# Performance work log

Hardware: AMD Instinct MI355X
Metric: run time of the kernel (lower is better)

The kernel has to match this reference:

```python
import jax, jax.numpy as jnp
import numpy as np

CUTOFF = 10.0
EPS_W = 1e-5
EPS_LN = 1e-5

def _silu(v):
    return v * jax.nn.sigmoid(v)

def setup_inputs() -> dict:
    key = jax.random.key(0)
    ks = jax.random.split(key, 12)
    N, E, H, R = 50000, 300000, 256, 64
    s = lambda fan_in: 1.0 / np.sqrt(fan_in)
    inp = {
        'x': jax.random.normal(ks[0], (N, H), jnp.float32),
        'edge_index': jax.random.randint(ks[1], (2, E), 0, N, jnp.int64 if jax.config.jax_enable_x64 else jnp.int32),
        'distances': jax.random.uniform(ks[2], (E,), jnp.float32) * CUTOFF,
        'centers': jnp.linspace(0.0, CUTOFF, R).astype(jnp.float32),
        'widths': jnp.full((R,), CUTOFF / R, jnp.float32),
        'rbf_w1': jax.random.normal(ks[3], (R, R), jnp.float32) * s(R),
        'rbf_b1': jnp.zeros((R,), jnp.float32),
        'rbf_w2': jax.random.normal(ks[4], (R, R), jnp.float32) * s(R),
        'rbf_b2': jnp.zeros((R,), jnp.float32),
        'filt_w1': jax.random.normal(ks[5], (R, H), jnp.float32) * s(R),
        'filt_b1': jnp.zeros((H,), jnp.float32),
        'filt_w2': jax.random.normal(ks[6], (H, H), jnp.float32) * s(H),
        'filt_b2': jnp.zeros((H,), jnp.float32),
        'filt_w3': jax.random.normal(ks[7], (H, H), jnp.float32) * s(H),
        'filt_b3': jnp.zeros((H,), jnp.float32),
        'node_w': jax.random.normal(ks[8], (H, H), jnp.float32) * s(H),
        'node_b': jnp.zeros((H,), jnp.float32),
        'ln_g': jnp.ones((H,), jnp.float32),
        'ln_b': jnp.zeros((H,), jnp.float32),
        'gate_w': jax.random.normal(ks[9], (H, H), jnp.float32) * s(H),
        'gate_b': jnp.zeros((H,), jnp.float32),
    }
    return inp

def reference(x, edge_index, distances, centers, widths,
              rbf_w1, rbf_b1, rbf_w2, rbf_b2,
              filt_w1, filt_b1, filt_w2, filt_b2, filt_w3, filt_b3,
              node_w, node_b, ln_g, ln_b, gate_w, gate_b):
    # LearnableRBF: envelope * gaussian basis, then 2-layer SiLU proj
    d = distances
    env = 0.5 * (jnp.cos(d * jnp.pi / CUTOFF) + 1.0) * (d < CUTOFF).astype(x.dtype)  # [E]
    rbf = jnp.exp(-0.5 * ((d[:, None] - centers) / (jnp.abs(widths) + EPS_W)) ** 2)   # [E,R]
    r = rbf * env[:, None]
    r = _silu(r @ rbf_w1 + rbf_b1) @ rbf_w2 + rbf_b2                                  # [E,R]
    # filter network: Lin-SiLU-Lin-SiLU-Lin
    W = _silu(r @ filt_w1 + filt_b1)
    W = _silu(W @ filt_w2 + filt_b2) @ filt_w3 + filt_b3                              # [E,H]
    # gather -> modulate -> scatter-add (CFConv messaging)
    row, col = edge_index[0], edge_index[1]
    msg = (x[col] @ node_w + node_b) * W                                              # [E,H]
    agg = jax.ops.segment_sum(msg, row, num_segments=x.shape[0])                      # [N,H]
    h = x + agg
    mu = jnp.mean(h, axis=-1, keepdims=True)
    var = jnp.var(h, axis=-1, keepdims=True)
    out = (h - mu) / jnp.sqrt(var + EPS_LN) * ln_g + ln_b
    return out * jax.nn.sigmoid(out @ gate_w + gate_b)
```

## Files before the change

### kernel.cpp

```cpp
#include <hip/hip_runtime.h>
#include <hip/hip_bf16.h>
#include <math.h>

typedef __attribute__((ext_vector_type(8))) short bf16x8;
typedef __attribute__((ext_vector_type(4))) float f32x4;
typedef unsigned short ushort_t;

constexpr float F_CUTOFF = 10.0f;
constexpr float F_EPS_W  = 1e-5f;
constexpr float F_EPS_LN = 1e-5f;
constexpr float F_PI     = 3.14159265358979323846f;

__device__ __forceinline__ float silu_f(float v)   { return v / (1.0f + __expf(-v)); }
__device__ __forceinline__ float sigmoid_f(float v){ return 1.0f / (1.0f + __expf(-v)); }

__device__ __forceinline__ ushort_t f2bf(float f) {
    union { __hip_bfloat16 h; ushort_t u; } v; v.h = __float2bfloat16(f); return v.u;
}
__device__ __forceinline__ float bf2f(ushort_t u) {
    union { unsigned u; float f; } v; v.u = ((unsigned)u) << 16; return v.f;
}

__global__ void count_kernel(const int* __restrict__ eidx, int* __restrict__ cnt, int E)
{
// ... 160 lines not shown
    float4 bv1 = reinterpret_cast<const float4*>(bias)[j04 + 1];
    float bb[8] = {bv0.x, bv0.y, bv0.z, bv0.w, bv1.x, bv1.y, bv1.z, bv1.w};

    #pragma unroll
    for (int r = 0; r < 8; ++r) {
        int row = row0 + r0 + r;
        if (row >= M) continue;
        ushort_t o8[8];
        #pragma unroll
        for (int c = 0; c < 8; ++c) o8[c] = f2bf(acc[r][c] + bb[c]);
        *reinterpret_cast<uint4*>(out + (size_t)row * 256 + jt * 8) = *reinterpret_cast<uint4*>(o8);
    }
}

__global__ __launch_bounds__(256)
void gate_gemm_kernel(const float* __restrict__ A, const float* __restrict__ Wm,
                      const float* __restrict__ bias, float* __restrict__ out, int M)
{
    __shared__ float4 As4[64][64];
    const int t = threadIdx.x;
    const int row0 = blockIdx.x * 64;

    #pragma unroll
    for (int i = 0; i < 16; ++i) {
        int flat = t + i * 256;
        int r = flat >> 6, k4 = flat & 63;
        int row = row0 + r;
        float4 v = make_float4(0.f, 0.f, 0.f, 0.f);
        if (row < M) v = reinterpret_cast<const float4*>(A)[row * 64 + k4];
        As4[r][k4] = v;
    }
    __syncthreads();

    const int jt  = t & 31;
    const int et  = t >> 5;
    const int j04 = jt * 2;
    const int r0  = et * 8;

    float acc[8][8];
    #pragma unroll
    for (int r = 0; r < 8; ++r)
        #pragma unroll
        for (int c = 0; c < 8; ++c) acc[r][c] = 0.f;

    for (int k4 = 0; k4 < 64; ++k4) {
        float4 a4[8];
        #pragma unroll
        for (int r = 0; r < 8; ++r) a4[r] = As4[r0 + r][k4];
        #pragma unroll
        for (int q = 0; q < 4; ++q) {
            const int k = k4 * 4 + q;
            float4 b0 = reinterpret_cast<const float4*>(Wm)[k * 64 + j04];
            float4 b1 = reinterpret_cast<const float4*>(Wm)[k * 64 + j04 + 1];
            float bb[8] = {b0.x, b0.y, b0.z, b0.w, b1.x, b1.y, b1.z, b1.w};
            float av;
            #pragma unroll
            for (int r = 0; r < 8; ++r) {
                av = (q == 0) ? a4[r].x : (q == 1) ? a4[r].y : (q == 2) ? a4[r].z : a4[r].w;
                #pragma unroll
                for (int c = 0; c < 8; ++c) acc[r][c] = fmaf(av, bb[c], acc[r][c]);
            }
        }
    }

    float4 bv0 = reinterpret_cast<const float4*>(bias)[j04];
    float4 bv1 = reinterpret_cast<const float4*>(bias)[j04 + 1];
    float bb[8] = {bv0.x, bv0.y, bv0.z, bv0.w, bv1.x, bv1.y, bv1.z, bv1.w};

    #pragma unroll
    for (int r = 0; r < 8; ++r) {
        int row = row0 + r0 + r;
        if (row >= M) continue;
        float4 a0 = As4[r0 + r][j04];
        float4 a1 = As4[r0 + r][j04 + 1];
        float aa[8] = {a0.x, a0.y, a0.z, a0.w, a1.x, a1.y, a1.z, a1.w};
        float o[8];
        #pragma unroll
        for (int c = 0; c < 8; ++c) o[c] = aa[c] * sigmoid_f(acc[r][c] + bb[c]);
        reinterpret_cast<float4*>(out)[row * 64 + j04]     = make_float4(o[0], o[1], o[2], o[3]);
        reinterpret_cast<float4*>(out)[row * 64 + j04 + 1] = make_float4(o[4], o[5], o[6], o[7]);
    }
}

__global__ __launch_bounds__(256)
void rbf_kernel(const float* __restrict__ distp,
                const float* __restrict__ centers, const float* __restrict__ widths,
                ushort_t* __restrict__ r, int Mc)
{
    int idx = blockIdx.x * 256 + threadIdx.x;
    if (idx >= Mc * 8) return;
    int e  = idx >> 3;
    int c0 = (idx & 7) * 8;
    float d = distp[e];
    float env = (d < F_CUTOFF) ? 0.5f * (__cosf(d * (F_PI / F_CUTOFF)) + 1.0f) : 0.0f;
    ushort_t o[8];
    #pragma unroll
    for (int i = 0; i < 8; ++i) {
        int n = c0 + i;
        float w = fabsf(widths[n]) + F_EPS_W;
        float z = (d - centers[n]) / w;
        o[i] = f2bf(env * __expf(-0.5f * z * z));
    }
    *reinterpret_cast<uint4*>(r + (size_t)e * 64 + c0) = *reinterpret_cast<uint4*>(o);
}

__global__ __launch_bounds__(256, 4)
void gemm_k64_kernel(const ushort_t* A, const ushort_t* __restrict__ Wt,
                     const float* __restrict__ bias, ushort_t* out, int M)
{
    __shared__ __align__(16) unsigned char sA[128 * 128];
    const int t = threadIdx.x;
    const int m0 = blockIdx.x * 128;
    const int w = t >> 6, lane = t & 63;
    const int g = lane >> 4, q = lane & 15;

    #pragma unroll
    for (int i = 0; i < 4; ++i) {
        int s = t + i * 256;
        int r = s >> 3, u = s & 7;
        int row = m0 + r; row = (row < M) ? row : (M - 1);
        uint4 v = *reinterpret_cast<const uint4*>(A + (size_t)row * 64 + ((u ^ (r & 7)) * 8));
        *reinterpret_cast<uint4*>(sA + s * 16) = v;
    }
    __syncthreads();

    f32x4 acc[2][4];
    #pragma unroll
    for (int mt = 0; mt < 2; ++mt)
        #pragma unroll
        for (int nt = 0; nt < 4; ++nt) acc[mt][nt] = (f32x4){0.f, 0.f, 0.f, 0.f};

    #pragma unroll
    for (int kk = 0; kk < 2; ++kk) {
        bf16x8 b[4];
        #pragma unroll
        for (int nt = 0; nt < 4; ++nt) {
            int n = nt * 16 + q;
            b[nt] = *reinterpret_cast<const bf16x8*>(Wt + n * 64 + kk * 32 + g * 8);
        }
        bf16x8 a[2];
        #pragma unroll
        for (int mt = 0; mt < 2; ++mt) {
            int m = w * 32 + mt * 16 + q;
            int unit = (4 * kk + g) ^ (m & 7);
            a[mt] = *reinterpret_cast<const bf16x8*>(sA + m * 128 + unit * 16);
        }
        #pragma unroll
        for (int mt = 0; mt < 2; ++mt)
            #pragma unroll
            for (int nt = 0; nt < 4; ++nt)
                acc[mt][nt] = __builtin_amdgcn_mfma_f32_16x16x32_bf16(a[mt], b[nt], acc[mt][nt], 0, 0, 0);
    }
    __syncthreads();

    const bool evenq = (q & 1) == 0;
    #pragma unroll
    for (int nt = 0; nt < 4; ++nt) {
        int n0  = nt * 16 + q;
        int n_e = n0 & ~1;
        float2 bv = *reinterpret_cast<const float2*>(bias + n_e);
        #pragma unroll
        for (int mt = 0; mt < 2; ++mt) {
            float v[4], p[4];
            #pragma unroll
            for (int r = 0; r < 4; ++r) { v[r] = acc[mt][nt][r]; p[r] = __shfl_xor(v[r], 1, 64); }
            #pragma unroll
            for (int rr = 0; rr < 2; ++rr) {
                int r = evenq ? rr : (2 + rr);
                float lo = silu_f((evenq ? v[r] : p[r]) + bv.x);
                float hi = silu_f((evenq ? p[r] : v[r]) + bv.y);
                int m = w * 32 + mt * 16 + 4 * g + r;
                unsigned u = (unsigned)f2bf(lo) | ((unsigned)f2bf(hi) << 16);
                *reinterpret_cast<unsigned*>(sA + m * 128 + n_e * 2) = u;
            }
        }
    }
    __syncthreads();

    {
        int row = t >> 1, j = t & 1;
        if (m0 + row < M) {
            #pragma unroll
            for (int i = 0; i < 4; ++i) {
                uint4 v = *reinterpret_cast<const uint4*>(sA + row * 128 + (j * 4 + i) * 16);
                *reinterpret_cast<uint4*>(out + (size_t)(m0 + row) * 64 + (j * 4 + i) * 8) = v;
            }
        }
    }
}

__global__ __launch_bounds__(256, 4)
void gemm_k64n256_kernel(const ushort_t* __restrict__ A, const ushort_t* __restrict__ Wt,
                         const float* __restrict__ bias, ushort_t* __restrict__ out, int M)
{
    __shared__ __align__(16) unsigned char sA[64 * 128];
    __shared__ __align__(16) unsigned char obuf[32 * 512];
    const int t = threadIdx.x;
    const int m0 = blockIdx.x * 64;
    const int wn = t >> 6, lane = t & 63;
    const int g = lane >> 4, q = lane & 15;

    #pragma unroll
    for (int i = 0; i < 2; ++i) {
        int s = t + i * 256;
        int r = s >> 3, u = s & 7;
        int row = m0 + r; row = (row < M) ? row : (M - 1);
        uint4 v = *reinterpret_cast<const uint4*>(A + (size_t)row * 64 + ((u ^ (r & 7)) * 8));
        *reinterpret_cast<uint4*>(sA + s * 16) = v;
    }
    __syncthreads();

    f32x4 acc[4][4];
    #pragma unroll
    for (int mt = 0; mt < 4; ++mt)
        #pragma unroll
        for (int nt = 0; nt < 4; ++nt) acc[mt][nt] = (f32x4){0.f, 0.f, 0.f, 0.f};

    #pragma unroll
    for (int kk = 0; kk < 2; ++kk) {
        bf16x8 b[4];
        #pragma unroll
        for (int nt = 0; nt < 4; ++nt) {
            int n = wn * 64 + nt * 16 + q;
            b[nt] = *reinterpret_cast<const bf16x8*>(Wt + n * 64 + kk * 32 + g * 8);
        }
        bf16x8 a[4];
        #pragma unroll
        for (int mt = 0; mt < 4; ++mt) {
            int m = mt * 16 + q;
            int unit = (4 * kk + g) ^ (m & 7);
            a[mt] = *reinterpret_cast<const bf16x8*>(sA + m * 128 + unit * 16);
        }
        #pragma unroll
        for (int mt = 0; mt < 4; ++mt)
            #pragma unroll
            for (int nt = 0; nt < 4; ++nt)
                acc[mt][nt] = __builtin_amdgcn_mfma_f32_16x16x32_bf16(a[mt], b[nt], acc[mt][nt], 0, 0, 0);
    }

    const bool evenq = (q & 1) == 0;
    #pragma unroll
    for (int half = 0; half < 2; ++half) {
        #pragma unroll
        for (int mtl = 0; mtl < 2; ++mtl) {
            int mt = half * 2 + mtl;
            #pragma unroll
            for (int nt = 0; nt < 4; ++nt) {
                int n0  = wn * 64 + nt * 16 + q;
                int n_e = n0 & ~1;
                float2 bv = *reinterpret_cast<const float2*>(bias + n_e);
                float v[4], p[4];
                #pragma unroll
                for (int r = 0; r < 4; ++r) { v[r] = acc[mt][nt][r]; p[r] = __shfl_xor(v[r], 1, 64); }
                #pragma unroll
                for (int rr = 0; rr < 2; ++rr) {
                    int r = evenq ? rr : (2 + rr);
                    float lo = silu_f((evenq ? v[r] : p[r]) + bv.x);
                    float hi = silu_f((evenq ? p[r] : v[r]) + bv.y);
                    int ml = mtl * 16 + 4 * g + r;
                    unsigned u = (unsigned)f2bf(lo) | ((unsigned)f2bf(hi) << 16);
                    *reinterpret_cast<unsigned*>(obuf + ml * 512 + n_e * 2) = u;
                }
            }
        }
        __syncthreads();
        {
            int row = t >> 3, c = t & 7;
            int grow = m0 + half * 32 + row;
            if (grow < M) {
                #pragma unroll
                for (int i = 0; i < 4; ++i) {
                    uint4 v = *reinterpret_cast<const uint4*>(obuf + row * 512 + (c + 8 * i) * 16);
                    *reinterpret_cast<uint4*>(out + (size_t)grow * 256 + (c + 8 * i) * 8) = v;
                }
            }
        }
        __syncthreads();
    }
}

template<bool SILU>
__global__ __launch_bounds__(256, 3)
void gemm_k256_kernel(const ushort_t* __restrict__ A, const ushort_t* __restrict__ Wt,
                      const float* __restrict__ bias, ushort_t* __restrict__ out, int M)
{
    __shared__ __align__(16) unsigned char sbuf[2][8192];

    const int t  = threadIdx.x;
    const int m0 = blockIdx.x * 64;
    const int wn   = t >> 6;
    const int lane = t & 63;
    const int g = lane >> 4, q = lane & 15;

    const int s0r = t >> 3,         s0u = t & 7;
    const int s1r = (t + 256) >> 3, s1u = t & 7;
    const ushort_t* src0base = A + (size_t)((m0 + s0r < M) ? (m0 + s0r) : (M - 1)) * 256 + ((s0u ^ (s0r & 7)) * 8);
    const ushort_t* src1base = A + (size_t)((m0 + s1r < M) ? (m0 + s1r) : (M - 1)) * 256 + ((s1u ^ (s1r & 7)) * 8);

    uint4 p0 = *reinterpret_cast<const uint4*>(src0base);
    uint4 p1 = *reinterpret_cast<const uint4*>(src1base);
    *reinterpret_cast<uint4*>(&sbuf[0][t * 16])         = p0;
    *reinterpret_cast<uint4*>(&sbuf[0][(t + 256) * 16]) = p1;
    __syncthreads();

    f32x4 acc[4][4];
    #pragma unroll
    for (int mt = 0; mt < 4; ++mt)
        #pragma unroll
        for (int nt = 0; nt < 4; ++nt) acc[mt][nt] = (f32x4){0.f, 0.f, 0.f, 0.f};

    for (int kt = 0; kt < 4; ++kt) {
        const int cur = kt & 1;
        uint4 nx0, nx1;
        if (kt < 3) {
            nx0 = *reinterpret_cast<const uint4*>(src0base + (kt + 1) * 64);
            nx1 = *reinterpret_cast<const uint4*>(src1base + (kt + 1) * 64);
        }
        #pragma unroll
        for (int ks = 0; ks < 2; ++ks) {
            bf16x8 b[4];
            #pragma unroll
            for (int nt = 0; nt < 4; ++nt) {
                int n = wn * 64 + nt * 16 + q;
                b[nt] = *reinterpret_cast<const bf16x8*>(Wt + (size_t)n * 256 + kt * 64 + ks * 32 + g * 8);
            }
            bf16x8 a[4];
            #pragma unroll
            for (int mt = 0; mt < 4; ++mt) {
                int r = mt * 16 + q;
                int u = (ks * 4 + g) ^ (r & 7);
                a[mt] = *reinterpret_cast<const bf16x8*>(&sbuf[cur][r * 128 + u * 16]);
            }
            #pragma unroll
            for (int mt = 0; mt < 4; ++mt)
                #pragma unroll
                for (int nt = 0; nt < 4; ++nt)
                    acc[mt][nt] = __builtin_amdgcn_mfma_f32_16x16x32_bf16(a[mt], b[nt], acc[mt][nt], 0, 0, 0);
        }
        __syncthreads();
        if (kt < 3) {
            *reinterpret_cast<uint4*>(&sbuf[cur ^ 1][t * 16])         = nx0;
            *reinterpret_cast<uint4*>(&sbuf[cur ^ 1][(t + 256) * 16]) = nx1;
            __syncthreads();
        }
    }

    unsigned char* obuf = &sbuf[0][0];
    const bool evenq = (q & 1) == 0;
    #pragma unroll
    for (int half = 0; half < 2; ++half) {
        __syncthreads();
        #pragma unroll
        for (int mtl = 0; mtl < 2; ++mtl) {
            int mt = half * 2 + mtl;
            #pragma unroll
            for (int nt = 0; nt < 4; ++nt) {
                int n0  = wn * 64 + nt * 16 + q;
                int n_e = n0 & ~1;
                float2 bv = *reinterpret_cast<const float2*>(bias + n_e);
                float v[4], p[4];
                #pragma unroll
                for (int r = 0; r < 4; ++r) { v[r] = acc[mt][nt][r]; p[r] = __shfl_xor(v[r], 1, 64); }
                #pragma unroll
                for (int rr = 0; rr < 2; ++rr) {
                    int r = evenq ? rr : (2 + rr);
// ... 41 lines not shown

    uint4 p0 = *reinterpret_cast<const uint4*>(src0base);
    uint4 p1 = *reinterpret_cast<const uint4*>(src1base);
    *reinterpret_cast<uint4*>(&sbuf[0][t * 16])         = p0;
    *reinterpret_cast<uint4*>(&sbuf[0][(t + 256) * 16]) = p1;
    __syncthreads();

    f32x4 acc[4][4];
    #pragma unroll
    for (int mt = 0; mt < 4; ++mt)
        #pragma unroll
        for (int nt = 0; nt < 4; ++nt) acc[mt][nt] = (f32x4){0.f, 0.f, 0.f, 0.f};

    for (int kt = 0; kt < 4; ++kt) {
        const int cur = kt & 1;
        uint4 nx0, nx1;
        if (kt < 3) {
            nx0 = *reinterpret_cast<const uint4*>(src0base + (kt + 1) * 64);
            nx1 = *reinterpret_cast<const uint4*>(src1base + (kt + 1) * 64);
        }
        #pragma unroll
        for (int ks = 0; ks < 2; ++ks) {
            bf16x8 b[4];
            #pragma unroll
            for (int nt = 0; nt < 4; ++nt) {
                int n = wn * 64 + nt * 16 + q;
                b[nt] = *reinterpret_cast<const bf16x8*>(Wt + (size_t)n * 256 + kt * 64 + ks * 32 + g * 8);
            }
            bf16x8 a[4];
            #pragma unroll
            for (int mt = 0; mt < 4; ++mt) {
                int r = mt * 16 + q;
                int u = (ks * 4 + g) ^ (r & 7);
                a[mt] = *reinterpret_cast<const bf16x8*>(&sbuf[cur][r * 128 + u * 16]);
            }
            #pragma unroll
            for (int mt = 0; mt < 4; ++mt)
                #pragma unroll
                for (int nt = 0; nt < 4; ++nt)
                    acc[mt][nt] = __builtin_amdgcn_mfma_f32_16x16x32_bf16(a[mt], b[nt], acc[mt][nt], 0, 0, 0);
        }
        __syncthreads();
        if (kt < 3) {
            *reinterpret_cast<uint4*>(&sbuf[cur ^ 1][t * 16])         = nx0;
            *reinterpret_cast<uint4*>(&sbuf[cur ^ 1][(t + 256) * 16]) = nx1;
            __syncthreads();
        }
    }

    float bn[4];
    #pragma unroll
    for (int nt = 0; nt < 4; ++nt) bn[nt] = bias[wn * 64 + nt * 16 + q];

    #pragma unroll
    for (int p = 0; p < 4; ++p) {
        #pragma unroll
        for (int nt = 0; nt < 4; ++nt) {
            int col = wn * 64 + nt * 16 + q;
            #pragma unroll
            for (int r = 0; r < 4; ++r) {
                int rl = 4 * g + r;
                obuf[rl][col] = sigmoid_f(acc[p][nt][r] + bn[nt]);
            }
        }
        __syncthreads();
        {
            int rl = t >> 4, c16 = t & 15;
            int grow = m0 + p * 16 + rl;
            if (grow < M) {
                float* orow = out + (size_t)grow * 256 + c16 * 16;
                #pragma unroll
                for (int i = 0; i < 4; ++i) {
                    float4 g4 = *reinterpret_cast<const float4*>(&obuf[rl][c16 * 16 + i * 4]);
                    float4 a4 = *reinterpret_cast<const float4*>(orow + i * 4);
                    a4.x *= g4.x; a4.y *= g4.y; a4.z *= g4.z; a4.w *= g4.w;
                    *reinterpret_cast<float4*>(orow + i * 4) = a4;
                }
            }
        }
        __syncthreads();
    }
}

__global__ __launch_bounds__(256, 3)
void fused_de_kernel(const ushort_t* A, const ushort_t* __restrict__ Wt2,
                     const float* __restrict__ b2,
                     const ushort_t* __restrict__ Wt3, const float* __restrict__ b3,
                     ushort_t* out, int M)
{
    __shared__ __align__(16) unsigned char sbuf[2][8192];
    __shared__ __align__(16) unsigned char f2l[64 * 512];

    const int t  = threadIdx.x;
    const int m0 = blockIdx.x * 64;
    const int wn   = t >> 6;
    const int lane = t & 63;
    const int g = lane >> 4, q = lane & 15;

    const int s0r = t >> 3,         s0u = t & 7;
    const int s1r = (t + 256) >> 3, s1u = t & 7;
    const ushort_t* src0base = A + (size_t)((m0 + s0r < M) ? (m0 + s0r) : (M - 1)) * 256 + ((s0u ^ (s0r & 7)) * 8);
    const ushort_t* src1base = A + (size_t)((m0 + s1r < M) ? (m0 + s1r) : (M - 1)) * 256 + ((s1u ^ (s1r & 7)) * 8);

    uint4 p0 = *reinterpret_cast<const uint4*>(src0base);
    uint4 p1 = *reinterpret_cast<const uint4*>(src1base);
    *reinterpret_cast<uint4*>(&sbuf[0][t * 16])         = p0;
    *reinterpret_cast<uint4*>(&sbuf[0][(t + 256) * 16]) = p1;
    __syncthreads();

    f32x4 acc[4][4];
    #pragma unroll
    for (int mt = 0; mt < 4; ++mt)
        #pragma unroll
        for (int nt = 0; nt < 4; ++nt) acc[mt][nt] = (f32x4){0.f, 0.f, 0.f, 0.f};

    for (int kt = 0; kt < 4; ++kt) {
        const int cur = kt & 1;
        uint4 nx0, nx1;
        if (kt < 3) {
            nx0 = *reinterpret_cast<const uint4*>(src0base + (kt + 1) * 64);
            nx1 = *reinterpret_cast<const uint4*>(src1base + (kt + 1) * 64);
        }
        #pragma unroll
        for (int ks = 0; ks < 2; ++ks) {
            bf16x8 b[4];
            #pragma unroll
            for (int nt = 0; nt < 4; ++nt) {
                int n = wn * 64 + nt * 16 + q;
                b[nt] = *reinterpret_cast<const bf16x8*>(Wt2 + (size_t)n * 256 + kt * 64 + ks * 32 + g * 8);
            }
            bf16x8 a[4];
            #pragma unroll
            for (int mt = 0; mt < 4; ++mt) {
                int r = mt * 16 + q;
                int u = (ks * 4 + g) ^ (r & 7);
                a[mt] = *reinterpret_cast<const bf16x8*>(&sbuf[cur][r * 128 + u * 16]);
            }
            #pragma unroll
            for (int mt = 0; mt < 4; ++mt)
                #pragma unroll
                for (int nt = 0; nt < 4; ++nt)
                    acc[mt][nt] = __builtin_amdgcn_mfma_f32_16x16x32_bf16(a[mt], b[nt], acc[mt][nt], 0, 0, 0);
        }
        __syncthreads();
        if (kt < 3) {
            *reinterpret_cast<uint4*>(&sbuf[cur ^ 1][t * 16])         = nx0;
            *reinterpret_cast<uint4*>(&sbuf[cur ^ 1][(t + 256) * 16]) = nx1;
            __syncthreads();
        }
    }

    const bool evenq = (q & 1) == 0;
    #pragma unroll
    for (int nt = 0; nt < 4; ++nt) {
        int n0  = wn * 64 + nt * 16 + q;
        int n_e = n0 & ~1;
        float2 bv = *reinterpret_cast<const float2*>(b2 + n_e);
        #pragma unroll
        for (int mt = 0; mt < 4; ++mt) {
            float v[4], p[4];
            #pragma unroll
            for (int r = 0; r < 4; ++r) { v[r] = acc[mt][nt][r]; p[r] = __shfl_xor(v[r], 1, 64); }
            #pragma unroll
            for (int rr = 0; rr < 2; ++rr) {
                int r = evenq ? rr : (2 + rr);
                float lo = silu_f((evenq ? v[r] : p[r]) + bv.x);
                float hi = silu_f((evenq ? p[r] : v[r]) + bv.y);
                int m = mt * 16 + 4 * g + r;
                unsigned u = (unsigned)f2bf(lo) | ((unsigned)f2bf(hi) << 16);
                int byte = m * 512 + (((n_e >> 3) ^ (m & 7)) << 4) + ((n_e & 7) * 2);
                *reinterpret_cast<unsigned*>(f2l + byte) = u;
            }
        }
    }
    __syncthreads();

    #pragma unroll
    for (int mt = 0; mt < 4; ++mt)
        #pragma unroll
        for (int nt = 0; nt < 4; ++nt) acc[mt][nt] = (f32x4){0.f, 0.f, 0.f, 0.f};

    #pragma unroll
    for (int kk = 0; kk < 8; ++kk) {
        bf16x8 b[4];
        #pragma unroll
        for (int nt = 0; nt < 4; ++nt) {
            int n = wn * 64 + nt * 16 + q;
            b[nt] = *reinterpret_cast<const bf16x8*>(Wt3 + (size_t)n * 256 + kk * 32 + g * 8);
        }
        bf16x8 a[4];
        #pragma unroll
        for (int mt = 0; mt < 4; ++mt) {
            int m = mt * 16 + q;
            int unit = (4 * kk + g) ^ (m & 7);
            a[mt] = *reinterpret_cast<const bf16x8*>(f2l + m * 512 + unit * 16);
        }
        #pragma unroll
        for (int mt = 0; mt < 4; ++mt)
            #pragma unroll
            for (int nt = 0; nt < 4; ++nt)
                acc[mt][nt] = __builtin_amdgcn_mfma_f32_16x16x32_bf16(a[mt], b[nt], acc[mt][nt], 0, 0, 0);
    }

    unsigned char* obuf = &sbuf[0][0];
    #pragma unroll
    for (int half = 0; half < 2; ++half) {
        __syncthreads();
        #pragma unroll
        for (int mtl = 0; mtl < 2; ++mtl) {
            int mt = half * 2 + mtl;
            #pragma unroll
            for (int nt = 0; nt < 4; ++nt) {
                int n0  = wn * 64 + nt * 16 + q;
                int n_e = n0 & ~1;
                float2 bv = *reinterpret_cast<const float2*>(b3 + n_e);
                float v[4], p[4];
                #pragma unroll
                for (int r = 0; r < 4; ++r) { v[r] = acc[mt][nt][r]; p[r] = __shfl_xor(v[r], 1, 64); }
                #pragma unroll
                for (int rr = 0; rr < 2; ++rr) {
                    int r = evenq ? rr : (2 + rr);
                    float lo = (evenq ? v[r] : p[r]) + bv.x;
                    float hi = (evenq ? p[r] : v[r]) + bv.y;
                    int ml = mtl * 16 + 4 * g + r;
                    unsigned u = (unsigned)f2bf(lo) | ((unsigned)f2bf(hi) << 16);
                    *reinterpret_cast<unsigned*>(obuf + ml * 512 + n_e * 2) = u;
                }
            }
        }
        __syncthreads();
        {
            int row = t >> 3, c = t & 7;
            int grow = m0 + half * 32 + row;
            if (grow < M) {
                #pragma unroll
                for (int i = 0; i < 4; ++i) {
                    uint4 v = *reinterpret_cast<const uint4*>(obuf + row * 512 + (c + 8 * i) * 16);
                    *reinterpret_cast<uint4*>(out + (size_t)grow * 256 + (c + 8 * i) * 8) = v;
                }
            }
        }
    }
}

__global__ __launch_bounds__(256)
void agg_node_kernel(const ushort_t* __restrict__ Wf, const int* __restrict__ colp,
                     const int* __restrict__ start, const ushort_t* __restrict__ y,
                     float* __restrict__ agg, int cs, int ce, int N)
{
    int lane = threadIdx.x & 63;
    int n    = blockIdx.x * 4 + (threadIdx.x >> 6);
    if (n >= N) return;
    int s0 = start[n], s1 = start[n + 1];
    if (s1 <= cs || s0 >= ce) return;
    int lo = (s0 > cs) ? s0 : cs;
    int hi = (s1 < ce) ? s1 : ce;

    float h0 = 0.f, h1 = 0.f, h2 = 0.f, h3 = 0.f;
    for (int s = lo; s < hi; ++s) {
        uint2 wv = *reinterpret_cast<const uint2*>(Wf + (size_t)(s - cs) * 256 + lane * 4);
        int c = colp[s];
        uint2 yv = *reinterpret_cast<const uint2*>(y + (size_t)c * 256 + lane * 4);
        h0 += bf2f((ushort_t)(wv.x & 0xffff)) * bf2f((ushort_t)(yv.x & 0xffff));
        h1 += bf2f((ushort_t)(wv.x >> 16))    * bf2f((ushort_t)(yv.x >> 16));
        h2 += bf2f((ushort_t)(wv.y & 0xffff)) * bf2f((ushort_t)(yv.y & 0xffff));
        h3 += bf2f((ushort_t)(wv.y >> 16))    * bf2f((ushort_t)(yv.y >> 16));
    }

    float* row = agg + (size_t)n * 256 + lane * 4;
    if (s0 >= cs && s1 <= ce) {
        *reinterpret_cast<float4*>(row) = make_float4(h0, h1, h2, h3);
    } else {
        unsafeAtomicAdd(&row[0], h0);
        unsafeAtomicAdd(&row[1], h1);
        unsafeAtomicAdd(&row[2], h2);
        unsafeAtomicAdd(&row[3], h3);
    }
}

template<int KS, int NT, bool SILU>
__device__ __forceinline__ void mlp_stage(const unsigned char* in, unsigned char* out,
                                          const ushort_t* __restrict__ Wt,
                                          const float* __restrict__ bias,
                                          int wn, int g, int q)
{
    constexpr int K = KS * 32;
    f32x4 acc[2][NT];
    #pragma unroll
    for (int mt = 0; mt < 2; ++mt)
        #pragma unroll
        for (int nt = 0; nt < NT; ++nt) acc[mt][nt] = (f32x4){0.f, 0.f, 0.f, 0.f};

    #pragma unroll
    for (int kk = 0; kk < KS; ++kk) {
        bf16x8 b[NT];
        #pragma unroll
        for (int nt = 0; nt < NT; ++nt) {
            int n = (wn * NT + nt) * 16 + q;
            b[nt] = *reinterpret_cast<const bf16x8*>(Wt + n * K + kk * 32 + g * 8);
        }
        bf16x8 a[2];
        #pragma unroll
        for (int mt = 0; mt < 2; ++mt) {
            int m = mt * 16 + q;
            int unit = (4 * kk + g) ^ (m & 7);
            a[mt] = *reinterpret_cast<const bf16x8*>(in + m * 512 + unit * 16);
        }
        #pragma unroll
        for (int mt = 0; mt < 2; ++mt)
            #pragma unroll
            for (int nt = 0; nt < NT; ++nt)
                acc[mt][nt] = __builtin_amdgcn_mfma_f32_16x16x32_bf16(a[mt], b[nt], acc[mt][nt], 0, 0, 0);
    }

    const bool evenq = (q & 1) == 0;
    #pragma unroll
    for (int nt = 0; nt < NT; ++nt) {
        int n0  = (wn * NT + nt) * 16 + q;
        int n_e = n0 & ~1;
        float2 bv = *reinterpret_cast<const float2*>(bias + n_e);
        #pragma unroll
        for (int mt = 0; mt < 2; ++mt) {
            float v[4], p[4];
            #pragma unroll
            for (int r = 0; r < 4; ++r) { v[r] = acc[mt][nt][r]; p[r] = __shfl_xor(v[r], 1, 64); }
// ... 185 lines not shown
    float4 h  = make_float4(hx.x + ha.x, hx.y + ha.y, hx.z + ha.z, hx.w + ha.w);
    float s  = h.x + h.y + h.z + h.w;
    float s2 = h.x * h.x + h.y * h.y + h.z * h.z + h.w * h.w;
    #pragma unroll
    for (int off = 32; off > 0; off >>= 1) {
        s  += __shfl_xor(s,  off, 64);
        s2 += __shfl_xor(s2, off, 64);
    }
    float mu  = s * (1.0f / 256.0f);
    float var = s2 * (1.0f / 256.0f) - mu * mu;
    float inv = rsqrtf(var + F_EPS_LN);
    float4 gv = reinterpret_cast<const float4*>(g)[lane];
    float4 bv = reinterpret_cast<const float4*>(b)[lane];
    float4 o;
    o.x = (h.x - mu) * inv * gv.x + bv.x;
    o.y = (h.y - mu) * inv * gv.y + bv.y;
    o.z = (h.z - mu) * inv * gv.z + bv.z;
    o.w = (h.w - mu) * inv * gv.w + bv.w;
    reinterpret_cast<float4*>(out0)[row * 64 + lane] = o;
    ushort_t ob[4] = {f2bf(o.x), f2bf(o.y), f2bf(o.z), f2bf(o.w)};
    *reinterpret_cast<uint2*>(out_bf + (size_t)row * 256 + lane * 4) = *reinterpret_cast<uint2*>(ob);
}

extern "C" void kernel_launch(void* const* d_in, const int* in_sizes, int n_in,
                              void* d_out, int out_size, void* d_ws, size_t ws_size,
                              hipStream_t stream)
{
    const float* x       = (const float*)d_in[0];
    const int*   eidx    = (const int*)  d_in[1];
    const float* dist    = (const float*)d_in[2];
    const float* centers = (const float*)d_in[3];
    const float* widths  = (const float*)d_in[4];
    const float* rbf_w1  = (const float*)d_in[5];
    const float* rbf_b1  = (const float*)d_in[6];
    const float* rbf_w2  = (const float*)d_in[7];
    const float* rbf_b2  = (const float*)d_in[8];
    const float* filt_w1 = (const float*)d_in[9];
    const float* filt_b1 = (const float*)d_in[10];
    const float* filt_w2 = (const float*)d_in[11];
    const float* filt_b2 = (const float*)d_in[12];
    const float* filt_w3 = (const float*)d_in[13];
    const float* filt_b3 = (const float*)d_in[14];
    const float* node_w  = (const float*)d_in[15];
    const float* node_b  = (const float*)d_in[16];
    const float* ln_g    = (const float*)d_in[17];
    const float* ln_b    = (const float*)d_in[18];
    const float* gate_w  = (const float*)d_in[19];
    const float* gate_b  = (const float*)d_in[20];

    const int N = in_sizes[0] / 256;
    const int E = in_sizes[2];

    char* wsb = (char*)d_ws;
    size_t off = 0;
    auto alloc = [&](size_t bytes, size_t align) -> char* {
        off = (off + align - 1) & ~(align - 1);
        char* p = wsb + off;
        off += bytes;
        return p;
    };
    ushort_t* y_bf   = (ushort_t*)alloc((size_t)N * 256 * 2, 16);
    ushort_t* wt1    = (ushort_t*)alloc(64 * 64 * 2, 16);
    ushort_t* wcomb  = (ushort_t*)alloc(256 * 64 * 2, 16);
    ushort_t* wf2t   = (ushort_t*)alloc(256 * 256 * 2, 16);
    ushort_t* wf3t   = (ushort_t*)alloc(256 * 256 * 2, 16);
    ushort_t* wnodet = (ushort_t*)alloc(256 * 256 * 2, 16);
    ushort_t* wgatet = (ushort_t*)alloc(256 * 256 * 2, 16);
    float*    bcomb  = (float*)   alloc(256 * 4, 16);
    int*      part   = (int*)     alloc(256 * 4, 16);
    int*      cnt    = (int*)     alloc((size_t)N * 4, 16);
    int*      start  = (int*)     alloc(((size_t)N + 1) * 4, 16);
    int*      colp   = (int*)     alloc((size_t)E * 4, 16);
    int*      nodep  = (int*)     alloc((size_t)E * 4, 16);
    float*    distp  = (float*)   alloc((size_t)E * 4, 256);

    size_t fixed_off = (off + 1023) & ~(size_t)1023;
    size_t avail = (ws_size > fixed_off) ? (ws_size - fixed_off) : 0;
    long Rl = (long)(avail / 640);
    int R = (int)(Rl & ~127L);
    int Eround = (E + 127) & ~127;
    if (R > Eround) R = Eround;
    const bool dense = (R >= 128) && ((E + R - 1) / R <= 8)
                       && ((size_t)R * 640 >= (size_t)N * 512 + 1024);
    ushort_t* rt_buf = (ushort_t*)(wsb + fixed_off);
    ushort_t* fw_buf = rt_buf + (size_t)R * 64;
    ushort_t* x_bf   = rt_buf;
    ushort_t* a_bf   = rt_buf;

    dim3 b256(256);
    const int range = (N + 255) / 256;

    cvt_transpose_kernel<<<dim3((64 * 64 + 255) / 256),   b256, 0, stream>>>(rbf_w1,  wt1, 64, 64, 6);
    combine_w_kernel<<<dim3(64), b256, 0, stream>>>(rbf_w2, filt_w1, wcomb);
    combine_b_kernel<<<dim3(1), b256, 0, stream>>>(rbf_b2, filt_w1, filt_b1, bcomb);
    cvt_transpose_kernel<<<dim3((256 * 256 + 255) / 256), b256, 0, stream>>>(filt_w2, wf2t, 256, 256, 8);
    cvt_transpose_kernel<<<dim3((256 * 256 + 255) / 256), b256, 0, stream>>>(filt_w3, wf3t, 256, 256, 8);
    cvt_transpose_kernel<<<dim3((256 * 256 + 255) / 256), b256, 0, stream>>>(node_w,  wnodet, 256, 256, 8);
    cvt_transpose_kernel<<<dim3((256 * 256 + 255) / 256), b256, 0, stream>>>(gate_w,  wgatet, 256, 256, 8);

    hipMemsetAsync(d_out, 0, (size_t)out_size * sizeof(float), stream);
    hipMemsetAsync(cnt, 0, (size_t)N * 4, stream);

    if (dense) {
        cast_bf16_kernel<<<dim3((N * 64 + 255) / 256), b256, 0, stream>>>(x, x_bf, (long)N * 64);
        gemm_k256_kernel<false><<<dim3((N + 63) / 64), b256, 0, stream>>>(
            x_bf, wnodet, node_b, y_bf, N);
    } else {
        gemm256_bf16_kernel<<<dim3((N + 63) / 64), b256, 0, stream>>>(x, node_w, node_b, y_bf, N);
    }

    count_kernel<<<dim3((E + 255) / 256), b256, 0, stream>>>(eidx, cnt, E);
    scan_sum_kernel<<<dim3(256), b256, 0, stream>>>(cnt, part, N, range);
    scan_write_kernel<<<dim3(1), b256, 0, stream>>>(part, cnt, start, N, range, E);
    scatter_kernel<<<dim3((E + 255) / 256), b256, 0, stream>>>(eidx, dist, cnt, colp, nodep, distp, E);

    if (dense) {
        for (int cs = 0; cs < E; cs += R) {
            int Mc = (E - cs < R) ? (E - cs) : R;
            rbf_kernel<<<dim3((Mc * 8 + 255) / 256), b256, 0, stream>>>(
                distp + cs, centers, widths, rt_buf, Mc);
            gemm_k64_kernel<<<dim3((Mc + 127) / 128), b256, 0, stream>>>(
                rt_buf, wt1, rbf_b1, rt_buf, Mc);
            gemm_k64n256_kernel<<<dim3((Mc + 63) / 64), b256, 0, stream>>>(
                rt_buf, wcomb, bcomb, fw_buf, Mc);
            fused_de_kernel<<<dim3((Mc + 63) / 64), b256, 0, stream>>>(
                fw_buf, wf2t, filt_b2, wf3t, filt_b3, fw_buf, Mc);
            agg_node_kernel<<<dim3((N + 3) / 4), b256, 0, stream>>>(
                fw_buf, colp, start, y_bf, (float*)d_out, cs, cs + Mc, N);
        }
        ln_kernel<<<dim3((N + 3) / 4), b256, 0, stream>>>(
            x, (float*)d_out, ln_g, ln_b, (float*)d_out, a_bf, N);
        gate_mfma_kernel<<<dim3((N + 63) / 64), b256, 0, stream>>>(
            a_bf, wgatet, gate_b, (float*)d_out, N);
    } else {
        edge_csr_kernel<<<dim3((E + 31) / 32), b256, 0, stream>>>(
            distp, colp, nodep, start, centers, widths,
            wt1, rbf_b1, wcomb, bcomb,
            wf2t, filt_b2, wf3t, filt_b3,
            y_bf, (float*)d_out, E);
        ln_kernel<<<dim3((N + 3) / 4), b256, 0, stream>>>(
            x, (float*)d_out, ln_g, ln_b, (float*)d_out, y_bf, N);
        gate_gemm_kernel<<<dim3((N + 63) / 64), b256, 0, stream>>>(
            (float*)d_out, gate_w, gate_b, (float*)d_out, N);
    }
}
```

Before: 894.3 us.

## Fuse RBF expansion into first GEMM and shrink fused filter kernel LDS

The RBF basis computation now happens directly inside the first K=64 GEMM's shared-memory load, so the separate rbf kernel launch and its bf16 round trip through global memory go away. The fused filter kernel drops its double-buffered A tile for a single buffer, and its epilogue writes in 16-row passes instead of 32-row halves. Together with raising launch bounds from 3 to 4 blocks per CU on the K=256 kernels, this cuts LDS use so more blocks can be resident. The cost is less load/compute overlap in the main loop and possible register pressure or spills under the tighter bound.

```diff
diff --git a/kernel.cpp b/kernel.cpp
--- a/kernel.cpp
+++ b/kernel.cpp
@@ -266,31 +266,11 @@
     }
 }
 
-__global__ __launch_bounds__(256)
-void rbf_kernel(const float* __restrict__ distp,
-                const float* __restrict__ centers, const float* __restrict__ widths,
-                ushort_t* __restrict__ r, int Mc)
-{
-    int idx = blockIdx.x * 256 + threadIdx.x;
-    if (idx >= Mc * 8) return;
-    int e  = idx >> 3;
-    int c0 = (idx & 7) * 8;
-    float d = distp[e];
-    float env = (d < F_CUTOFF) ? 0.5f * (__cosf(d * (F_PI / F_CUTOFF)) + 1.0f) : 0.0f;
-    ushort_t o[8];
-    #pragma unroll
-    for (int i = 0; i < 8; ++i) {
-        int n = c0 + i;
-        float w = fabsf(widths[n]) + F_EPS_W;
-        float z = (d - centers[n]) / w;
-        o[i] = f2bf(env * __expf(-0.5f * z * z));
-    }
-    *reinterpret_cast<uint4*>(r + (size_t)e * 64 + c0) = *reinterpret_cast<uint4*>(o);
-}
-
 __global__ __launch_bounds__(256, 4)
-void gemm_k64_kernel(const ushort_t* A, const ushort_t* __restrict__ Wt,
-                     const float* __restrict__ bias, ushort_t* out, int M)
+void rbf_t1_kernel(const float* __restrict__ distp,
+                   const float* __restrict__ centers, const float* __restrict__ widths,
+                   const ushort_t* __restrict__ Wt, const float* __restrict__ bias,
+                   ushort_t* __restrict__ out, int M)
 {
     __shared__ __align__(16) unsigned char sA[128 * 128];
     const int t = threadIdx.x;
@@ -302,9 +282,19 @@
     for (int i = 0; i < 4; ++i) {
         int s = t + i * 256;
         int r = s >> 3, u = s & 7;
-        int row = m0 + r; row = (row < M) ? row : (M - 1);
-        uint4 v = *reinterpret_cast<const uint4*>(A + (size_t)row * 64 + ((u ^ (r & 7)) * 8));
-        *reinterpret_cast<uint4*>(sA + s * 16) = v;
+        int row = m0 + r;
+        float d = (row < M) ? distp[row] : F_CUTOFF;
+        float env = (d < F_CUTOFF) ? 0.5f * (__cosf(d * (F_PI / F_CUTOFF)) + 1.0f) : 0.0f;
+        int c0 = (u ^ (r & 7)) * 8;
+        ushort_t o[8];
+        #pragma unroll
+        for (int j = 0; j < 8; ++j) {
+            int n = c0 + j;
+            float wd = fabsf(widths[n]) + F_EPS_W;
+            float z = (d - centers[n]) / wd;
+            o[j] = f2bf(env * __expf(-0.5f * z * z));
+        }
+        *reinterpret_cast<uint4*>(sA + s * 16) = *reinterpret_cast<uint4*>(o);
     }
     __syncthreads();
 
@@ -464,7 +454,7 @@
 }
 
 template<bool SILU>
-__global__ __launch_bounds__(256, 3)
+__global__ __launch_bounds__(256, 4)
 void gemm_k256_kernel(const ushort_t* __restrict__ A, const ushort_t* __restrict__ Wt,
                       const float* __restrict__ bias, ushort_t* __restrict__ out, int M)
 {
@@ -672,13 +662,13 @@
     }
 }
 
-__global__ __launch_bounds__(256, 3)
+__global__ __launch_bounds__(256, 4)
 void fused_de_kernel(const ushort_t* A, const ushort_t* __restrict__ Wt2,
                      const float* __restrict__ b2,
                      const ushort_t* __restrict__ Wt3, const float* __restrict__ b3,
                      ushort_t* out, int M)
 {
-    __shared__ __align__(16) unsigned char sbuf[2][8192];
+    __shared__ __align__(16) unsigned char sbuf[8192];
     __shared__ __align__(16) unsigned char f2l[64 * 512];
 
     const int t  = threadIdx.x;
@@ -694,8 +684,8 @@
 
     uint4 p0 = *reinterpret_cast<const uint4*>(src0base);
     uint4 p1 = *reinterpret_cast<const uint4*>(src1base);
-    *reinterpret_cast<uint4*>(&sbuf[0][t * 16])         = p0;
-    *reinterpret_cast<uint4*>(&sbuf[0][(t + 256) * 16]) = p1;
+    *reinterpret_cast<uint4*>(&sbuf[t * 16])         = p0;
+    *reinterpret_cast<uint4*>(&sbuf[(t + 256) * 16]) = p1;
     __syncthreads();
 
     f32x4 acc[4][4];
@@ -705,7 +695,6 @@
         for (int nt = 0; nt < 4; ++nt) acc[mt][nt] = (f32x4){0.f, 0.f, 0.f, 0.f};
 
     for (int kt = 0; kt < 4; ++kt) {
-        const int cur = kt & 1;
         uint4 nx0, nx1;
         if (kt < 3) {
             nx0 = *reinterpret_cast<const uint4*>(src0base + (kt + 1) * 64);
@@ -724,7 +713,7 @@
             for (int mt = 0; mt < 4; ++mt) {
                 int r = mt * 16 + q;
                 int u = (ks * 4 + g) ^ (r & 7);
-                a[mt] = *reinterpret_cast<const bf16x8*>(&sbuf[cur][r * 128 + u * 16]);
+                a[mt] = *reinterpret_cast<const bf16x8*>(&sbuf[r * 128 + u * 16]);
             }
             #pragma unroll
             for (int mt = 0; mt < 4; ++mt)
@@ -734,8 +723,8 @@
         }
         __syncthreads();
         if (kt < 3) {
-            *reinterpret_cast<uint4*>(&sbuf[cur ^ 1][t * 16])         = nx0;
-            *reinterpret_cast<uint4*>(&sbuf[cur ^ 1][(t + 256) * 16]) = nx1;
+            *reinterpret_cast<uint4*>(&sbuf[t * 16])         = nx0;
+            *reinterpret_cast<uint4*>(&sbuf[(t + 256) * 16]) = nx1;
             __syncthreads();
         }
     }
@@ -791,45 +780,40 @@
             for (int nt = 0; nt < 4; ++nt)
                 acc[mt][nt] = __builtin_amdgcn_mfma_f32_16x16x32_bf16(a[mt], b[nt], acc[mt][nt], 0, 0, 0);
     }
-
-    unsigned char* obuf = &sbuf[0][0];
-    #pragma unroll
-    for (int half = 0; half < 2; ++half) {
-        __syncthreads();
-        #pragma unroll
-        for (int mtl = 0; mtl < 2; ++mtl) {
-            int mt = half * 2 + mtl;
-            #pragma unroll
-            for (int nt = 0; nt < 4; ++nt) {
-                int n0  = wn * 64 + nt * 16 + q;
-                int n_e = n0 & ~1;
-                float2 bv = *reinterpret_cast<const float2*>(b3 + n_e);
-                float v[4], p[4];
-                #pragma unroll
-                for (int r = 0; r < 4; ++r) { v[r] = acc[mt][nt][r]; p[r] = __shfl_xor(v[r], 1, 64); }
-                #pragma unroll
-                for (int rr = 0; rr < 2; ++rr) {
-                    int r = evenq ? rr : (2 + rr);
-                    float lo = (evenq ? v[r] : p[r]) + bv.x;
-                    float hi = (evenq ? p[r] : v[r]) + bv.y;
-                    int ml = mtl * 16 + 4 * g + r;
-                    unsigned u = (unsigned)f2bf(lo) | ((unsigned)f2bf(hi) << 16);
-                    *reinterpret_cast<unsigned*>(obuf + ml * 512 + n_e * 2) = u;
-                }
+    __syncthreads();
+
+    #pragma unroll
+    for (int p = 0; p < 4; ++p) {
+        #pragma unroll
+        for (int nt = 0; nt < 4; ++nt) {
+            int n0  = wn * 64 + nt * 16 + q;
+            int n_e = n0 & ~1;
+            float2 bv = *reinterpret_cast<const float2*>(b3 + n_e);
+            float v[4], pp[4];
+            #pragma unroll
+            for (int r = 0; r < 4; ++r) { v[r] = acc[p][nt][r]; pp[r] = __shfl_xor(v[r], 1, 64); }
+            #pragma unroll
+            for (int rr = 0; rr < 2; ++rr) {
+                int r = evenq ? rr : (2 + rr);
+                float lo = (evenq ? v[r] : pp[r]) + bv.x;
+                float hi = (evenq ? pp[r] : v[r]) + bv.y;
+                int rl = 4 * g + r;
+                unsigned u = (unsigned)f2bf(lo) | ((unsigned)f2bf(hi) << 16);
+                *reinterpret_cast<unsigned*>(&sbuf[rl * 512 + n_e * 2]) = u;
             }
         }
         __syncthreads();
         {
-            int row = t >> 3, c = t & 7;
-            int grow = m0 + half * 32 + row;
+            int rl = t >> 4, c2 = t & 15;
+            int grow = m0 + p * 16 + rl;
             if (grow < M) {
-                #pragma unroll
-                for (int i = 0; i < 4; ++i) {
-                    uint4 v = *reinterpret_cast<const uint4*>(obuf + row * 512 + (c + 8 * i) * 16);
-                    *reinterpret_cast<uint4*>(out + (size_t)grow * 256 + (c + 8 * i) * 8) = v;
-                }
-            }
-        }
+                uint4 v0 = *reinterpret_cast<const uint4*>(&sbuf[rl * 512 + c2 * 32]);
+                uint4 v1 = *reinterpret_cast<const uint4*>(&sbuf[rl * 512 + c2 * 32 + 16]);
+                *reinterpret_cast<uint4*>(out + (size_t)grow * 256 + c2 * 16)     = v0;
+                *reinterpret_cast<uint4*>(out + (size_t)grow * 256 + c2 * 16 + 8) = v1;
+            }
+        }
+        __syncthreads();
     }
 }
 
@@ -1217,10 +1201,8 @@
     if (dense) {
         for (int cs = 0; cs < E; cs += R) {
             int Mc = (E - cs < R) ? (E - cs) : R;
-            rbf_kernel<<<dim3((Mc * 8 + 255) / 256), b256, 0, stream>>>(
-                distp + cs, centers, widths, rt_buf, Mc);
-            gemm_k64_kernel<<<dim3((Mc + 127) / 128), b256, 0, stream>>>(
-                rt_buf, wt1, rbf_b1, rt_buf, Mc);
+            rbf_t1_kernel<<<dim3((Mc + 127) / 128), b256, 0, stream>>>(
+                distp + cs, centers, widths, wt1, rbf_b1, rt_buf, Mc);
             gemm_k64n256_kernel<<<dim3((Mc + 63) / 64), b256, 0, stream>>>(
                 rt_buf, wcomb, bcomb, fw_buf, Mc);
             fused_de_kernel<<<dim3((Mc + 63) / 64), b256, 0, stream>>>(
```

Result: no change. 899.8 us (+0.6%).

## Fuse RBF into first GEMM and aggregation with LayerNorm for single-chunk path

Applied to the files above, without the earlier changes.

Computes the Gaussian RBF features directly into shared memory inside the first K=64 GEMM, so the separate RBF kernel and its write and read of the basis buffer are removed. When all edges fit in one chunk, aggregation is fused with the residual add and LayerNorm in a register-resident kernel, which also drops the output memset and the separate LN pass. The launch bound hint on the K=256 GEMM is also raised from 3 to 4 blocks. The single-chunk path only runs when the workspace is large enough to hold all edges at once.

```diff
diff --git a/kernel.cpp b/kernel.cpp
--- a/kernel.cpp
+++ b/kernel.cpp
@@ -266,31 +266,11 @@
     }
 }
 
-__global__ __launch_bounds__(256)
-void rbf_kernel(const float* __restrict__ distp,
-                const float* __restrict__ centers, const float* __restrict__ widths,
-                ushort_t* __restrict__ r, int Mc)
-{
-    int idx = blockIdx.x * 256 + threadIdx.x;
-    if (idx >= Mc * 8) return;
-    int e  = idx >> 3;
-    int c0 = (idx & 7) * 8;
-    float d = distp[e];
-    float env = (d < F_CUTOFF) ? 0.5f * (__cosf(d * (F_PI / F_CUTOFF)) + 1.0f) : 0.0f;
-    ushort_t o[8];
-    #pragma unroll
-    for (int i = 0; i < 8; ++i) {
-        int n = c0 + i;
-        float w = fabsf(widths[n]) + F_EPS_W;
-        float z = (d - centers[n]) / w;
-        o[i] = f2bf(env * __expf(-0.5f * z * z));
-    }
-    *reinterpret_cast<uint4*>(r + (size_t)e * 64 + c0) = *reinterpret_cast<uint4*>(o);
-}
-
 __global__ __launch_bounds__(256, 4)
-void gemm_k64_kernel(const ushort_t* A, const ushort_t* __restrict__ Wt,
-                     const float* __restrict__ bias, ushort_t* out, int M)
+void rbf_t1_kernel(const float* __restrict__ distp,
+                   const float* __restrict__ centers, const float* __restrict__ widths,
+                   const ushort_t* __restrict__ Wt, const float* __restrict__ bias,
+                   ushort_t* __restrict__ out, int M)
 {
     __shared__ __align__(16) unsigned char sA[128 * 128];
     const int t = threadIdx.x;
@@ -302,9 +282,19 @@
     for (int i = 0; i < 4; ++i) {
         int s = t + i * 256;
         int r = s >> 3, u = s & 7;
-        int row = m0 + r; row = (row < M) ? row : (M - 1);
-        uint4 v = *reinterpret_cast<const uint4*>(A + (size_t)row * 64 + ((u ^ (r & 7)) * 8));
-        *reinterpret_cast<uint4*>(sA + s * 16) = v;
+        int row = m0 + r;
+        float d = (row < M) ? distp[row] : F_CUTOFF;
+        float env = (d < F_CUTOFF) ? 0.5f * (__cosf(d * (F_PI / F_CUTOFF)) + 1.0f) : 0.0f;
+        int c0 = (u ^ (r & 7)) * 8;
+        ushort_t o[8];
+        #pragma unroll
+        for (int j = 0; j < 8; ++j) {
+            int n = c0 + j;
+            float wd = fabsf(widths[n]) + F_EPS_W;
+            float z = (d - centers[n]) / wd;
+            o[j] = f2bf(env * __expf(-0.5f * z * z));
+        }
+        *reinterpret_cast<uint4*>(sA + s * 16) = *reinterpret_cast<uint4*>(o);
     }
     __syncthreads();
 
@@ -464,7 +454,7 @@
 }
 
 template<bool SILU>
-__global__ __launch_bounds__(256, 3)
+__global__ __launch_bounds__(256, 4)
 void gemm_k256_kernel(const ushort_t* __restrict__ A, const ushort_t* __restrict__ Wt,
                       const float* __restrict__ bias, ushort_t* __restrict__ out, int M)
 {
@@ -831,6 +821,52 @@
             }
         }
     }
+}
+
+__global__ __launch_bounds__(256)
+void agg_ln_node_kernel(const ushort_t* __restrict__ Wf, const int* __restrict__ colp,
+                        const int* __restrict__ start, const ushort_t* __restrict__ y,
+                        const float* __restrict__ x,
+                        const float* __restrict__ gg, const float* __restrict__ bb,
+                        float* __restrict__ out0, ushort_t* __restrict__ out_bf, int N)
+{
+    int lane = threadIdx.x & 63;
+    int n    = blockIdx.x * 4 + (threadIdx.x >> 6);
+    if (n >= N) return;
+    int s0 = start[n], s1 = start[n + 1];
+
+    float4 hx = reinterpret_cast<const float4*>(x)[n * 64 + lane];
+    float h0 = hx.x, h1 = hx.y, h2 = hx.z, h3 = hx.w;
+    for (int s = s0; s < s1; ++s) {
+        uint2 wv = *reinterpret_cast<const uint2*>(Wf + (size_t)s * 256 + lane * 4);
+        int c = colp[s];
+        uint2 yv = *reinterpret_cast<const uint2*>(y + (size_t)c * 256 + lane * 4);
+        h0 += bf2f((ushort_t)(wv.x & 0xffff)) * bf2f((ushort_t)(yv.x & 0xffff));
+        h1 += bf2f((ushort_t)(wv.x >> 16))    * bf2f((ushort_t)(yv.x >> 16));
+        h2 += bf2f((ushort_t)(wv.y & 0xffff)) * bf2f((ushort_t)(yv.y & 0xffff));
+        h3 += bf2f((ushort_t)(wv.y >> 16))    * bf2f((ushort_t)(yv.y >> 16));
+    }
+
+    float su = h0 + h1 + h2 + h3;
+    float s2 = h0 * h0 + h1 * h1 + h2 * h2 + h3 * h3;
+    #pragma unroll
+    for (int off = 32; off > 0; off >>= 1) {
+        su += __shfl_xor(su, off, 64);
+        s2 += __shfl_xor(s2, off, 64);
+    }
+    float mu  = su * (1.0f / 256.0f);
+    float var = s2 * (1.0f / 256.0f) - mu * mu;
+    float inv = rsqrtf(var + F_EPS_LN);
+    float4 gv = reinterpret_cast<const float4*>(gg)[lane];
+    float4 bv = reinterpret_cast<const float4*>(bb)[lane];
+    float4 o;
+    o.x = (h0 - mu) * inv * gv.x + bv.x;
+    o.y = (h1 - mu) * inv * gv.y + bv.y;
+    o.z = (h2 - mu) * inv * gv.z + bv.z;
+    o.w = (h3 - mu) * inv * gv.w + bv.w;
+    reinterpret_cast<float4*>(out0)[n * 64 + lane] = o;
+    ushort_t ob[4] = {f2bf(o.x), f2bf(o.y), f2bf(o.z), f2bf(o.w)};
+    *reinterpret_cast<uint2*>(out_bf + (size_t)n * 256 + lane * 4) = *reinterpret_cast<uint2*>(ob);
 }
 
 __global__ __launch_bounds__(256)
@@ -1182,6 +1218,7 @@
     if (R > Eround) R = Eround;
     const bool dense = (R >= 128) && ((E + R - 1) / R <= 8)
                        && ((size_t)R * 640 >= (size_t)N * 512 + 1024);
+    const int nchunks = dense ? ((E + R - 1) / R) : 0;
     ushort_t* rt_buf = (ushort_t*)(wsb + fixed_off);
     ushort_t* fw_buf = rt_buf + (size_t)R * 64;
     ushort_t* x_bf   = rt_buf;
@@ -1198,7 +1235,6 @@
     cvt_transpose_kernel<<<dim3((256 * 256 + 255) / 256), b256, 0, stream>>>(node_w,  wnodet, 256, 256, 8);
     cvt_transpose_kernel<<<dim3((256 * 256 + 255) / 256), b256, 0, stream>>>(gate_w,  wgatet, 256, 256, 8);
 
-    hipMemsetAsync(d_out, 0, (size_t)out_size * sizeof(float), stream);
     hipMemsetAsync(cnt, 0, (size_t)N * 4, stream);
 
     if (dense) {
@@ -1215,24 +1251,33 @@
     scatter_kernel<<<dim3((E + 255) / 256), b256, 0, stream>>>(eidx, dist, cnt, colp, nodep, distp, E);
 
     if (dense) {
+        if (nchunks > 1)
+            hipMemsetAsync(d_out, 0, (size_t)out_size * sizeof(float), stream);
+
         for (int cs = 0; cs < E; cs += R) {
             int Mc = (E - cs < R) ? (E - cs) : R;
-            rbf_kernel<<<dim3((Mc * 8 + 255) / 256), b256, 0, stream>>>(
-                distp + cs, centers, widths, rt_buf, Mc);
-            gemm_k64_kernel<<<dim3((Mc + 127) / 128), b256, 0, stream>>>(
-                rt_buf, wt1, rbf_b1, rt_buf, Mc);
+            rbf_t1_kernel<<<dim3((Mc + 127) / 128), b256, 0, stream>>>(
+                distp + cs, centers, widths, wt1, rbf_b1, rt_buf, Mc);
             gemm_k64n256_kernel<<<dim3((Mc + 63) / 64), b256, 0, stream>>>(
                 rt_buf, wcomb, bcomb, fw_buf, Mc);
             fused_de_kernel<<<dim3((Mc + 63) / 64), b256, 0, stream>>>(
                 fw_buf, wf2t, filt_b2, wf3t, filt_b3, fw_buf, Mc);
-            agg_node_kernel<<<dim3((N + 3) / 4), b256, 0, stream>>>(
-                fw_buf, colp, start, y_bf, (float*)d_out, cs, cs + Mc, N);
-        }
-        ln_kernel<<<dim3((N + 3) / 4), b256, 0, stream>>>(
-            x, (float*)d_out, ln_g, ln_b, (float*)d_out, a_bf, N);
+            if (nchunks == 1) {
+                agg_ln_node_kernel<<<dim3((N + 3) / 4), b256, 0, stream>>>(
+                    fw_buf, colp, start, y_bf, x, ln_g, ln_b, (float*)d_out, a_bf, N);
+            } else {
+                agg_node_kernel<<<dim3((N + 3) / 4), b256, 0, stream>>>(
+                    fw_buf, colp, start, y_bf, (float*)d_out, cs, cs + Mc, N);
+            }
+        }
+        if (nchunks > 1) {
+            ln_kernel<<<dim3((N + 3) / 4), b256, 0, stream>>>(
+                x, (float*)d_out, ln_g, ln_b, (float*)d_out, a_bf, N);
+        }
         gate_mfma_kernel<<<dim3((N + 63) / 64), b256, 0, stream>>>(
             a_bf, wgatet, gate_b, (float*)d_out, N);
     } else {
+        hipMemsetAsync(d_out, 0, (size_t)out_size * sizeof(float), stream);
         edge_csr_kernel<<<dim3((E + 31) / 32), b256, 0, stream>>>(
             distp, colp, nodep, start, centers, widths,
             wt1, rbf_b1, wcomb, bcomb,
```

Measured after the change: 853.3 us. 1.05x faster.
